# Performance work log

Measured on AMD Instinct MI355X. Metric: run time of the kernel, lower is better.

Reference implementation:

```python
import jax, jax.numpy as jnp
import numpy as np

N = 30000   # nodes
E = 600000  # edges
IN = 256    # in_channels
HID = 128   # 2*out_channels
OUT = 64    # out_channels


def setup_inputs() -> dict:
    key = jax.random.key(0)
    k = jax.random.split(key, 6)
    x = jax.random.normal(k[0], (N, IN), dtype=jnp.float32)
    edge_index = jax.random.randint(k[1], (2, E), 0, N, dtype=jnp.int64)
    W1 = jax.random.normal(k[2], (IN, HID), dtype=jnp.float32) * (1.0 / np.sqrt(IN))
    b1 = jnp.zeros((HID,), dtype=jnp.float32)
    W2 = jax.random.normal(k[3], (HID, OUT), dtype=jnp.float32) * (1.0 / np.sqrt(HID))
    b2 = jnp.zeros((OUT,), dtype=jnp.float32)
    return {"x": x, "edge_index": edge_index, "W1": W1, "b1": b1, "W2": W2, "b2": b2}


def _gcn_norm(edge_index, n_nodes):
    # PyG gcn_norm with add_self_loops=True, edge_weight=1
    loop = jnp.arange(n_nodes, dtype=edge_index.dtype)
    src = jnp.concatenate([edge_index[0], loop])
    dst = jnp.concatenate([edge_index[1], loop])
    deg = jax.ops.segment_sum(jnp.ones_like(dst, dtype=jnp.float32), dst,
                              num_segments=n_nodes)
    dinv = jnp.where(deg > 0, jax.lax.rsqrt(deg), 0.0)
    norm = dinv[src] * dinv[dst]  # [E+N]
    return src, dst, norm


def _gcn_conv(h, src, dst, norm, W, b, n_nodes):
    h = h @ W                              # [N, out] linear first (PyG order)
    msg = h[src] * norm[:, None]           # gather + per-edge scale, [E+N, out]
    out = jax.ops.segment_sum(msg, dst, num_segments=n_nodes)  # scatter-add
    return out + b


def reference(x, edge_index, W1, b1, W2, b2):
    n_nodes = x.shape[0]
    src, dst, norm = _gcn_norm(edge_index, n_nodes)
    h = _gcn_conv(x, src, dst, norm, W1, b1, n_nodes)
    h = jax.nn.relu(h)
    return _gcn_conv(h, src, dst, norm, W2, b2, n_nodes)
```

## Files before the change

kernel.cpp:

```cpp
#include <hip/hip_runtime.h>


#define GCN_IN 256
#define GCN_HID 128
#define GCN_OUT 64

#define BKT 128
#define SBE 4096
#define SRCM 0x1FFFFFFu

typedef unsigned short ushort_t;
typedef __attribute__((ext_vector_type(8))) short short8;
typedef __attribute__((ext_vector_type(8))) unsigned short ushort8;
typedef __attribute__((ext_vector_type(4))) float f32x4;

__device__ inline float bf2f(ushort_t u) {
  union { unsigned int i; float f; } x; x.i = ((unsigned int)u) << 16; return x.f;
}
__device__ inline ushort_t f2bf(float f) {
  union { float f; unsigned int i; } u; u.f = f;
  unsigned int r = u.i + 0x7FFFu + ((u.i >> 16) & 1u);
  return (ushort_t)(r >> 16);
}

__global__ void probe_kernel(const ushort_t* __restrict__ xu,
                             const int* __restrict__ ei,
                             int* __restrict__ flags) {
  int lane = threadIdx.x;
  int c = 0, nz = 0;
  for (int i = lane; i < 128; i += 64) {
    ushort_t u = xu[2 * i];
    int e = (u >> 7) & 0xFF;
    c += (e >= 100 && e <= 140) ? 1 : 0;
    nz += (ei[2 * i + 1] != 0) ? 1 : 0;
  }
  for (int off = 32; off > 0; off >>= 1) {
    c += __shfl_down(c, off);
    nz += __shfl_down(nz, off);
  }
  if (lane == 0) {
    flags[0] = (c >= 64) ? 0 : 1;
    flags[1] = (nz == 0) ? 1 : 0;
  }
}

__global__ void hist_kernel(const int* __restrict__ ei, int E,
                            int* __restrict__ Hmat, int nsb, int nbin,
                            const int* __restrict__ flags) {
  __shared__ int hist[256];
  int t = threadIdx.x;
  int sb = blockIdx.x;
  hist[t] = 0;
  __syncthreads();
  int base = sb * SBE;
  int end = base + SBE; if (end > E) end = E;
  bool i64 = flags[1] != 0;
  for (int i = base + t; i < end; i += 256) {
    int d = i64 ? ei[2 * E + 2 * i] : ei[E + i];
    atomicAdd(&hist[d >> 7], 1);
  }
  __syncthreads();
  for (int b = t; b < nbin; b += 256)
    Hmat[b * nsb + sb] = hist[b];
}

__global__ void scanA_kernel(const int* __restrict__ Hmat, int nsb,
                             int* __restrict__ binsum) {
  __shared__ int red[256];
  int t = threadIdx.x;
  const int* row = Hmat + (size_t)blockIdx.x * nsb;
  int s = 0;
  for (int i = t; i < nsb; i += 256) s += row[i];
  red[t] = s;
  __syncthreads();
  for (int off = 128; off > 0; off >>= 1) {
    if (t < off) red[t] += red[t + off];
    __syncthreads();
  }
  if (t == 0) binsum[blockIdx.x] = red[0];
}

__global__ void scanC_kernel(int* __restrict__ Hmat, int nsb,
                             const int* __restrict__ binsum, int nbin) {
  __shared__ int bred[256];
  __shared__ int red[256];
  int t = threadIdx.x;
  int bs = (t < nbin) ? binsum[t] : 0;
  bred[t] = bs;
  __syncthreads();
  for (int off = 1; off < 256; off <<= 1) {
    int u = (t >= off) ? bred[t - off] : 0;
    __syncthreads();
    bred[t] += u;
    __syncthreads();
  }
  __shared__ int seed_sh;
  if (t == (int)blockIdx.x) seed_sh = bred[t] - bs;
  __syncthreads();
  int seed = seed_sh;
  int* row = Hmat + (size_t)blockIdx.x * nsb;
  int self = (t < nsb) ? row[t] : 0;
  red[t] = self;
  __syncthreads();
  for (int off = 1; off < 256; off <<= 1) {
    int u = (t >= off) ? red[t - off] : 0;
    __syncthreads();
    red[t] += u;
    __syncthreads();
  }
  if (t < nsb) row[t] = seed + red[t] - self;
}

__global__ void stage2_kernel(const int* __restrict__ ei, int E,
                              const int* __restrict__ Hscan, int nsb, int nbin,
                              unsigned int* __restrict__ stage,
                              const int* __restrict__ flags) {
  __shared__ int cur[256];
  int t = threadIdx.x;
  int sb = blockIdx.x;
  for (int b = t; b < nbin; b += 256)
    cur[b] = Hscan[b * nsb + sb];
  __syncthreads();
  int base = sb * SBE;
  int end = base + SBE; if (end > E) end = E;
  bool i64 = flags[1] != 0;
  for (int i = base + t; i < end; i += 256) {
    int s, d;
    if (i64) { s = ei[2 * i]; d = ei[2 * E + 2 * i]; }
    else     { s = ei[i];     d = ei[E + i]; }
    int pos = atomicAdd(&cur[d >> 7], 1);
    stage[pos] = (unsigned int)s | ((unsigned int)(d & 127) << 25);
  }
}

__global__ void scatter_kernel(const unsigned int* __restrict__ stage,
                               const int* __restrict__ Hmat, int nsb, int nbin,
                               int* __restrict__ csr_src,
                               int* __restrict__ row_ptr,
                               float* __restrict__ dinv, int n, int E) {
  __shared__ int lcnt[BKT];
  __shared__ int lscan[BKT];
  __shared__ int lcur[BKT];
  const int t = threadIdx.x;
  const int b = blockIdx.x;
  const int node0 = b * BKT;
  const int nn = (n - node0 < BKT) ? (n - node0) : BKT;
  const int rb = Hmat[b * nsb];
  const int re = (b + 1 < nbin) ? Hmat[(b + 1) * nsb] : E;
  if (t < BKT) lcnt[t] = 0;
  __syncthreads();
  for (int i = rb + t; i < re; i += 256)
    atomicAdd(&lcnt[stage[i] >> 25], 1);
  __syncthreads();
  if (t < BKT) lscan[t] = lcnt[t];
  __syncthreads();
  for (int off = 1; off < BKT; off <<= 1) {
    int v = 0;
    if (t < BKT && t >= off) v = lscan[t - off];
    __syncthreads();
    if (t < BKT) lscan[t] += v;
    __syncthreads();
  }
  if (t < BKT) {
    int excl = rb + lscan[t] - lcnt[t];
    lcur[t] = excl;
    if (t < nn) {
      row_ptr[node0 + t] = excl;
      dinv[node0 + t] = rsqrtf((float)(lcnt[t] + 1));
    }
  }
  if (t == 0 && node0 + nn == n) row_ptr[n] = E;
  __syncthreads();
  for (int i = rb + t; i < re; i += 256) {
    unsigned int p = stage[i];
    int l = p >> 25;
    int pos = atomicAdd(&lcur[l], 1);
    csr_src[pos] = (int)(p & SRCM);
  }
}

__global__ void prep_w_kernel(const void* __restrict__ W1, const void* __restrict__ W2,
                              ushort_t* __restrict__ Wt1, ushort_t* __restrict__ Wt2,
                              const int* __restrict__ flags) {
  int i = blockIdx.x * blockDim.x + threadIdx.x;
  bool f32 = flags[0] != 0;
  if (i < GCN_IN * GCN_HID) {
    int k = i >> 7, n = i & 127;
    float v = f32 ? ((const float*)W1)[i] : bf2f(((const ushort_t*)W1)[i]);
    Wt1[n * GCN_IN + k] = f2bf(v);
  }
  int j = i - GCN_IN * GCN_HID;
  if (j >= 0 && j < GCN_HID * GCN_OUT) {
    int k = j >> 6, n = j & 63;
    float v = f32 ? ((const float*)W2)[j] : bf2f(((const ushort_t*)W2)[j]);
    Wt2[n * GCN_HID + k] = f2bf(v);
  }
}

template<int K, int NC, int A_MODE>
__global__ __launch_bounds__(256)
void gemm_mfma_kernel(const void* __restrict__ A, const ushort_t* __restrict__ Bt,
                      ushort_t* __restrict__ C, int M, const int* __restrict__ flags) {
  constexpr int KT = 32;
  constexpr int NT = NC / 32;
  __shared__ ushort_t As[32 * KT];
  __shared__ ushort_t Bs[NC * KT];
  const int tid = threadIdx.x;
  const int wv = tid >> 6;
  const int lane = tid & 63;
  const int ml = lane & 15;
  const int quad = lane >> 4;
  const int row0 = blockIdx.x * 32;
  const int mrow = (wv & 1) * 16 + ml;
  const int ncol0 = (wv >> 1) * (NC / 2);
  const bool aF32 = (A_MODE == 0) && (flags[0] != 0);
  f32x4 acc[NT] = {};

  for (int kt = 0; kt < K; kt += KT) {
    for (int c = tid; c < 32 * KT / 8; c += 256) {
      int r = c >> 2, cq = c & 3;
      ushort8 o;
      if (row0 + r < M) {
        if (aF32) {
          const float* ap = (const float*)A + (size_t)(row0 + r) * K + kt + cq * 8;
          float4 f0 = *(const float4*)ap;
          float4 f1 = *(const float4*)(ap + 4);
          o[0] = f2bf(f0.x); o[1] = f2bf(f0.y); o[2] = f2bf(f0.z); o[3] = f2bf(f0.w);
          o[4] = f2bf(f1.x); o[5] = f2bf(f1.y); o[6] = f2bf(f1.z); o[7] = f2bf(f1.w);
        } else {
          o = *(const ushort8*)((const ushort_t*)A + (size_t)(row0 + r) * K + kt + cq * 8);
        }
      } else {
        o = (ushort8)0;
      }
      *(ushort8*)&As[c * 8] = o;
    }
    for (int c = tid; c < NC * KT / 8; c += 256) {
      int n = c >> 2, cq = c & 3;
      *(ushort8*)&Bs[c * 8] = *(const ushort8*)(Bt + (size_t)n * K + kt + cq * 8);
    }
    __syncthreads();
    short8 af = *(const short8*)&As[mrow * KT + quad * 8];
#pragma unroll
    for (int t = 0; t < NT; ++t) {
      short8 bf = *(const short8*)&Bs[(ncol0 + t * 16 + ml) * KT + quad * 8];
      acc[t] = __builtin_amdgcn_mfma_f32_16x16x32_bf16(af, bf, acc[t], 0, 0, 0);
    }
    __syncthreads();
  }

  const int orow = row0 + (wv & 1) * 16 + quad * 4;
#pragma unroll
  for (int t = 0; t < NT; ++t) {
    int col = ncol0 + t * 16 + ml;
#pragma unroll
    for (int r = 0; r < 4; ++r) {
      if (orow + r < M)
        C[(size_t)(orow + r) * NC + col] = f2bf(acc[t][r]);
    }
  }
}


__global__ void aggregate_relu_kernel(const ushort_t* __restrict__ h,
                                      const int* __restrict__ row_ptr,
                                      const int* __restrict__ csr_src,
                                      const float* __restrict__ dinv,
                                      const void* __restrict__ bias,
                                      ushort_t* __restrict__ outp, int n,
                                      const int* __restrict__ flags) {
  int wave = threadIdx.x >> 6;
  int lane = threadIdx.x & 63;
  int v = blockIdx.x * (blockDim.x >> 6) + wave;
  if (v >= n) return;
  const int q = lane & 15, g = lane >> 4;
  float acc[8] = {};
  int beg = row_ptr[v], end = row_ptr[v + 1];
  for (int base = beg; base < end; base += 64) {
    int navail = end - base; if (navail > 64) navail = 64;
    int sv = 0; float dv = 0.f;
    if (base + lane < end) { sv = csr_src[base + lane]; dv = dinv[sv]; }
    for (int j = 0; j < navail; j += 4) {
      int e = j + g;
      int s = __shfl(sv, e);
      float ds = __shfl(dv, e);
      ushort8 hv = *(const ushort8*)(h + (size_t)s * GCN_HID + q * 8);
#pragma unroll
      for (int k = 0; k < 8; ++k) acc[k] = fmaf(ds, bf2f(hv[k]), acc[k]);
    }
  }
#pragma unroll
  for (int k = 0; k < 8; ++k) {
    acc[k] += __shfl_xor(acc[k], 16);
    acc[k] += __shfl_xor(acc[k], 32);
  }
  if (g == 0) {
    float di = dinv[v];
    float sl = di * di;
    ushort8 hv = *(const ushort8*)(h + (size_t)v * GCN_HID + q * 8);
    const bool bF32 = flags[0] != 0;
    ushort8 o;
#pragma unroll
    for (int k = 0; k < 8; ++k) {
      float bv = bF32 ? ((const float*)bias)[q * 8 + k]
                      : bf2f(((const ushort_t*)bias)[q * 8 + k]);
      o[k] = f2bf(fmaxf(di * acc[k] + sl * bf2f(hv[k]) + bv, 0.f));
    }
    *(ushort8*)(outp + (size_t)v * GCN_HID + q * 8) = o;
  }
}

__global__ void aggregate_out_kernel(const ushort_t* __restrict__ h,
                                     const int* __restrict__ row_ptr,
                                     const int* __restrict__ csr_src,
                                     const float* __restrict__ dinv,
                                     const void* __restrict__ bias,
                                     void* __restrict__ outp, int n,
                                     const int* __restrict__ flags) {
  int wave = threadIdx.x >> 6;
  int lane = threadIdx.x & 63;
  int v = blockIdx.x * (blockDim.x >> 6) + wave;
  if (v >= n) return;
  const int q = lane & 7, g = lane >> 3;
  float acc[8] = {};
  int beg = row_ptr[v], end = row_ptr[v + 1];
  for (int base = beg; base < end; base += 64) {
    int navail = end - base; if (navail > 64) navail = 64;
    int sv = 0; float dv = 0.f;
    if (base + lane < end) { sv = csr_src[base + lane]; dv = dinv[sv]; }
    for (int j = 0; j < navail; j += 8) {
      int e = j + g;
      int s = __shfl(sv, e);
      float ds = __shfl(dv, e);
      ushort8 hv = *(const ushort8*)(h + (size_t)s * GCN_OUT + q * 8);
#pragma unroll
      for (int k = 0; k < 8; ++k) acc[k] = fmaf(ds, bf2f(hv[k]), acc[k]);
    }
  }
#pragma unroll
  for (int k = 0; k < 8; ++k) {
    acc[k] += __shfl_xor(acc[k], 8);
    acc[k] += __shfl_xor(acc[k], 16);
    acc[k] += __shfl_xor(acc[k], 32);
  }
  if (g == 0) {
    float di = dinv[v];
    float sl = di * di;
    ushort8 hv = *(const ushort8*)(h + (size_t)v * GCN_OUT + q * 8);
    const bool oF32 = flags[0] != 0;
    float r[8];
#pragma unroll
    for (int k = 0; k < 8; ++k) {
      float bv = oF32 ? ((const float*)bias)[q * 8 + k]
                      : bf2f(((const ushort_t*)bias)[q * 8 + k]);
      r[k] = di * acc[k] + sl * bf2f(hv[k]) + bv;
    }
    if (oF32) {
      float* op = (float*)outp + (size_t)v * GCN_OUT + q * 8;
      *(float4*)op = make_float4(r[0], r[1], r[2], r[3]);
      *(float4*)(op + 4) = make_float4(r[4], r[5], r[6], r[7]);
    } else {
      ushort8 o;
#pragma unroll
      for (int k = 0; k < 8; ++k) o[k] = f2bf(r[k]);
      *(ushort8*)((ushort_t*)outp + (size_t)v * GCN_OUT + q * 8) = o;
    }
  }
}


extern "C" void kernel_launch(void* const* d_in, const int* in_sizes, int n_in,
                              void* d_out, int out_size, void* d_ws, size_t ws_size,
                              hipStream_t stream) {
  const void* x  = d_in[0];
  const int*  ei = (const int*)d_in[1];
  const void* W1 = d_in[2];
  const void* b1 = d_in[3];
  const void* W2 = d_in[4];
  const void* b2 = d_in[5];

  const int N = in_sizes[0] / GCN_IN;
  const int E = in_sizes[1] / 2;
  const int nsb  = (E + SBE - 1) / SBE;
  const int nbin = (N + BKT - 1) / BKT;

  size_t off = 0;
  auto alloc = [&](size_t bytes) -> void* {
    void* p = (char*)d_ws + off;
    off += (bytes + 255) & ~(size_t)255;
    return p;
  };
  int*          flags   = (int*)alloc(256);
  int*          binsum  = (int*)alloc(256 * 4);
  int*          Hmat    = (int*)alloc((size_t)nbin * nsb * 4);
  unsigned int* stage   = (unsigned int*)alloc((size_t)E * 4);
  int*          csr_src = (int*)alloc((size_t)E * 4);
  int*          row_ptr = (int*)alloc((size_t)(N + 1) * 4);
  float*        dinv    = (float*)alloc((size_t)N * 4);
  ushort_t*     h1      = (ushort_t*)alloc((size_t)N * GCN_HID * 2);
  ushort_t*     hag     = (ushort_t*)alloc((size_t)N * GCN_HID * 2);
  ushort_t*     wt1     = (ushort_t*)alloc((size_t)GCN_HID * GCN_IN * 2);
  ushort_t*     wt2     = (ushort_t*)alloc((size_t)GCN_OUT * GCN_HID * 2);
  ushort_t*     h2      = h1;

  probe_kernel<<<1, 64, 0, stream>>>((const ushort_t*)x, ei, flags);
  hist_kernel<<<nsb, 256, 0, stream>>>(ei, E, Hmat, nsb, nbin, flags);
  scanA_kernel<<<nbin, 256, 0, stream>>>(Hmat, nsb, binsum);
  scanC_kernel<<<nbin, 256, 0, stream>>>(Hmat, nsb, binsum, nbin);
  stage2_kernel<<<nsb, 256, 0, stream>>>(ei, E, Hmat, nsb, nbin, stage, flags);
  scatter_kernel<<<nbin, 256, 0, stream>>>(stage, Hmat, nsb, nbin, csr_src,
                                           row_ptr, dinv, N, E);

  prep_w_kernel<<<(GCN_IN * GCN_HID + GCN_HID * GCN_OUT + 255) / 256, 256, 0, stream>>>(
      W1, W2, wt1, wt2, flags);

  gemm_mfma_kernel<GCN_IN, GCN_HID, 0>
      <<<(N + 31) / 32, 256, 0, stream>>>(x, wt1, h1, N, flags);

  int gAgg = (N + 3) / 4;
  aggregate_relu_kernel<<<gAgg, 256, 0, stream>>>(h1, row_ptr, csr_src,
                                                  dinv, b1, hag, N, flags);

  gemm_mfma_kernel<GCN_HID, GCN_OUT, 2>
      <<<(N + 31) / 32, 256, 0, stream>>>(hag, wt2, h2, N, flags);

  aggregate_out_kernel<<<gAgg, 256, 0, stream>>>(h2, row_ptr, csr_src,
                                                 dinv, b2, d_out, N, flags);
}
```

Before: 177.1 us.

## Fold dtype probes into consumers, merge scan kernels, swizzle GEMM LDS, unroll gathers

Removes the separate probe kernel: each kernel that needs the int64 or fp32 check now recomputes it inline, with the fp32 check moved into prep_w using W1. The two scan kernels are merged into one that recomputes bin sums per block and writes a separate Hscan buffer. The GEMM now stages K in chunks of up to 128 with an XOR-swizzled LDS layout, cutting the number of barriers. Both aggregation loops are unrolled to issue four independent gathers per step for more memory-level parallelism. The trade-off is redundant per-block probe and bin-sum work plus higher register pressure in the aggregation kernels.

```diff
diff --git a/kernel.cpp b/kernel.cpp
--- a/kernel.cpp
+++ b/kernel.cpp
@@ -23,38 +23,20 @@
   return (ushort_t)(r >> 16);
 }
 
-__global__ void probe_kernel(const ushort_t* __restrict__ xu,
-                             const int* __restrict__ ei,
-                             int* __restrict__ flags) {
-  int lane = threadIdx.x;
-  int c = 0, nz = 0;
-  for (int i = lane; i < 128; i += 64) {
-    ushort_t u = xu[2 * i];
-    int e = (u >> 7) & 0xFF;
-    c += (e >= 100 && e <= 140) ? 1 : 0;
-    nz += (ei[2 * i + 1] != 0) ? 1 : 0;
-  }
-  for (int off = 32; off > 0; off >>= 1) {
-    c += __shfl_down(c, off);
-    nz += __shfl_down(nz, off);
-  }
-  if (lane == 0) {
-    flags[0] = (c >= 64) ? 0 : 1;
-    flags[1] = (nz == 0) ? 1 : 0;
-  }
-}
-
 __global__ void hist_kernel(const int* __restrict__ ei, int E,
-                            int* __restrict__ Hmat, int nsb, int nbin,
-                            const int* __restrict__ flags) {
+                            int* __restrict__ Hmat, int nsb, int nbin) {
   __shared__ int hist[256];
+  __shared__ int nzc;
   int t = threadIdx.x;
   int sb = blockIdx.x;
   hist[t] = 0;
-  __syncthreads();
+  if (t == 0) nzc = 0;
+  __syncthreads();
+  if (t < 128 && ei[2 * t + 1] != 0) atomicAdd(&nzc, 1);
+  __syncthreads();
+  bool i64 = (nzc == 0);
   int base = sb * SBE;
   int end = base + SBE; if (end > E) end = E;
-  bool i64 = flags[1] != 0;
   for (int i = base + t; i < end; i += 256) {
     int d = i64 ? ei[2 * E + 2 * i] : ei[E + i];
     atomicAdd(&hist[d >> 7], 1);
@@ -64,28 +46,17 @@
     Hmat[b * nsb + sb] = hist[b];
 }
 
-__global__ void scanA_kernel(const int* __restrict__ Hmat, int nsb,
-                             int* __restrict__ binsum) {
-  __shared__ int red[256];
-  int t = threadIdx.x;
-  const int* row = Hmat + (size_t)blockIdx.x * nsb;
-  int s = 0;
-  for (int i = t; i < nsb; i += 256) s += row[i];
-  red[t] = s;
-  __syncthreads();
-  for (int off = 128; off > 0; off >>= 1) {
-    if (t < off) red[t] += red[t + off];
-    __syncthreads();
-  }
-  if (t == 0) binsum[blockIdx.x] = red[0];
-}
-
-__global__ void scanC_kernel(int* __restrict__ Hmat, int nsb,
-                             const int* __restrict__ binsum, int nbin) {
+__global__ void scanAC_kernel(const int* __restrict__ Hmat,
+                              int* __restrict__ Hscan, int nsb, int nbin) {
   __shared__ int bred[256];
   __shared__ int red[256];
+  __shared__ int seed_sh;
   int t = threadIdx.x;
-  int bs = (t < nbin) ? binsum[t] : 0;
+  int bs = 0;
+  if (t < nbin) {
+    const int* row = Hmat + (size_t)t * nsb;
+    for (int i = 0; i < nsb; ++i) bs += row[i];
+  }
   bred[t] = bs;
   __syncthreads();
   for (int off = 1; off < 256; off <<= 1) {
@@ -94,11 +65,10 @@
     bred[t] += u;
     __syncthreads();
   }
-  __shared__ int seed_sh;
   if (t == (int)blockIdx.x) seed_sh = bred[t] - bs;
   __syncthreads();
   int seed = seed_sh;
-  int* row = Hmat + (size_t)blockIdx.x * nsb;
+  const int* row = Hmat + (size_t)blockIdx.x * nsb;
   int self = (t < nsb) ? row[t] : 0;
   red[t] = self;
   __syncthreads();
@@ -108,22 +78,25 @@
     red[t] += u;
     __syncthreads();
   }
-  if (t < nsb) row[t] = seed + red[t] - self;
+  if (t < nsb) Hscan[(size_t)blockIdx.x * nsb + t] = seed + red[t] - self;
 }
 
 __global__ void stage2_kernel(const int* __restrict__ ei, int E,
                               const int* __restrict__ Hscan, int nsb, int nbin,
-                              unsigned int* __restrict__ stage,
-                              const int* __restrict__ flags) {
+                              unsigned int* __restrict__ stage) {
   __shared__ int cur[256];
+  __shared__ int nzc;
   int t = threadIdx.x;
   int sb = blockIdx.x;
+  if (t == 0) nzc = 0;
+  __syncthreads();
+  if (t < 128 && ei[2 * t + 1] != 0) atomicAdd(&nzc, 1);
   for (int b = t; b < nbin; b += 256)
     cur[b] = Hscan[b * nsb + sb];
   __syncthreads();
+  bool i64 = (nzc == 0);
   int base = sb * SBE;
   int end = base + SBE; if (end > E) end = E;
-  bool i64 = flags[1] != 0;
   for (int i = base + t; i < end; i += 256) {
     int s, d;
     if (i64) { s = ei[2 * i]; d = ei[2 * E + 2 * i]; }
@@ -134,7 +107,7 @@
 }
 
 __global__ void scatter_kernel(const unsigned int* __restrict__ stage,
-                               const int* __restrict__ Hmat, int nsb, int nbin,
+                               const int* __restrict__ Hscan, int nsb, int nbin,
                                int* __restrict__ csr_src,
                                int* __restrict__ row_ptr,
                                float* __restrict__ dinv, int n, int E) {
@@ -145,8 +118,8 @@
   const int b = blockIdx.x;
   const int node0 = b * BKT;
   const int nn = (n - node0 < BKT) ? (n - node0) : BKT;
-  const int rb = Hmat[b * nsb];
-  const int re = (b + 1 < nbin) ? Hmat[(b + 1) * nsb] : E;
+  const int rb = Hscan[b * nsb];
+  const int re = (b + 1 < nbin) ? Hscan[(b + 1) * nsb] : E;
   if (t < BKT) lcnt[t] = 0;
   __syncthreads();
   for (int i = rb + t; i < re; i += 256)
@@ -181,9 +154,20 @@
 
 __global__ void prep_w_kernel(const void* __restrict__ W1, const void* __restrict__ W2,
                               ushort_t* __restrict__ Wt1, ushort_t* __restrict__ Wt2,
-                              const int* __restrict__ flags) {
+                              int* __restrict__ flags) {
+  __shared__ int csh;
+  if (threadIdx.x == 0) csh = 0;
+  __syncthreads();
+  if (threadIdx.x < 128) {
+    ushort_t u = ((const ushort_t*)W1)[2 * threadIdx.x];
+    int e = (u >> 7) & 0xFF;
+    if (e >= 100 && e <= 140) atomicAdd(&csh, 1);
+  }
+  __syncthreads();
+  bool f32 = (csh < 64);
+  if (blockIdx.x == 0 && threadIdx.x == 0) flags[0] = f32 ? 1 : 0;
+
   int i = blockIdx.x * blockDim.x + threadIdx.x;
-  bool f32 = flags[0] != 0;
   if (i < GCN_IN * GCN_HID) {
     int k = i >> 7, n = i & 127;
     float v = f32 ? ((const float*)W1)[i] : bf2f(((const ushort_t*)W1)[i]);
@@ -201,10 +185,11 @@
 __global__ __launch_bounds__(256)
 void gemm_mfma_kernel(const void* __restrict__ A, const ushort_t* __restrict__ Bt,
                       ushort_t* __restrict__ C, int M, const int* __restrict__ flags) {
-  constexpr int KT = 32;
+  constexpr int KH = (K > 128) ? 128 : K;
+  constexpr int KPC = KH / 8;
   constexpr int NT = NC / 32;
-  __shared__ ushort_t As[32 * KT];
-  __shared__ ushort_t Bs[NC * KT];
+  __shared__ ushort_t As[32 * KH];
+  __shared__ ushort_t Bs[NC * KH];
   const int tid = threadIdx.x;
   const int wv = tid >> 6;
   const int lane = tid & 63;
@@ -216,37 +201,46 @@
   const bool aF32 = (A_MODE == 0) && (flags[0] != 0);
   f32x4 acc[NT] = {};
 
-  for (int kt = 0; kt < K; kt += KT) {
-    for (int c = tid; c < 32 * KT / 8; c += 256) {
-      int r = c >> 2, cq = c & 3;
+  for (int ch = 0; ch < K; ch += KH) {
+    if (ch) __syncthreads();
+    for (int c = tid; c < 32 * KPC; c += 256) {
+      int r = c / KPC, cq = c % KPC;
       ushort8 o;
       if (row0 + r < M) {
         if (aF32) {
-          const float* ap = (const float*)A + (size_t)(row0 + r) * K + kt + cq * 8;
+          const float* ap = (const float*)A + (size_t)(row0 + r) * K + ch + cq * 8;
           float4 f0 = *(const float4*)ap;
           float4 f1 = *(const float4*)(ap + 4);
           o[0] = f2bf(f0.x); o[1] = f2bf(f0.y); o[2] = f2bf(f0.z); o[3] = f2bf(f0.w);
           o[4] = f2bf(f1.x); o[5] = f2bf(f1.y); o[6] = f2bf(f1.z); o[7] = f2bf(f1.w);
         } else {
-          o = *(const ushort8*)((const ushort_t*)A + (size_t)(row0 + r) * K + kt + cq * 8);
+          o = *(const ushort8*)((const ushort_t*)A + (size_t)(row0 + r) * K + ch + cq * 8);
         }
       } else {
         o = (ushort8)0;
       }
-      *(ushort8*)&As[c * 8] = o;
-    }
-    for (int c = tid; c < NC * KT / 8; c += 256) {
-      int n = c >> 2, cq = c & 3;
-      *(ushort8*)&Bs[c * 8] = *(const ushort8*)(Bt + (size_t)n * K + kt + cq * 8);
-    }
-    __syncthreads();
-    short8 af = *(const short8*)&As[mrow * KT + quad * 8];
-#pragma unroll
-    for (int t = 0; t < NT; ++t) {
-      short8 bf = *(const short8*)&Bs[(ncol0 + t * 16 + ml) * KT + quad * 8];
-      acc[t] = __builtin_amdgcn_mfma_f32_16x16x32_bf16(af, bf, acc[t], 0, 0, 0);
-    }
-    __syncthreads();
+      int byte = (cq * 16) ^ ((r & 7) << 4);
+      *(ushort8*)((char*)As + r * (KH * 2) + byte) = o;
+    }
+    for (int c = tid; c < NC * KPC; c += 256) {
+      int nr = c / KPC, cq = c % KPC;
+      ushort8 o = *(const ushort8*)(Bt + (size_t)nr * K + ch + cq * 8);
+      int byte = (cq * 16) ^ ((nr & 7) << 4);
+      *(ushort8*)((char*)Bs + nr * (KH * 2) + byte) = o;
+    }
+    __syncthreads();
+#pragma unroll
+    for (int kt = 0; kt < KH; kt += 32) {
+      int abyte = (kt * 2 + quad * 16) ^ ((mrow & 7) << 4);
+      short8 af = *(const short8*)((const char*)As + mrow * (KH * 2) + abyte);
+#pragma unroll
+      for (int t = 0; t < NT; ++t) {
+        int nr = ncol0 + t * 16 + ml;
+        int bbyte = (kt * 2 + quad * 16) ^ ((nr & 7) << 4);
+        short8 bf = *(const short8*)((const char*)Bs + nr * (KH * 2) + bbyte);
+        acc[t] = __builtin_amdgcn_mfma_f32_16x16x32_bf16(af, bf, acc[t], 0, 0, 0);
+      }
+    }
   }
 
   const int orow = row0 + (wv & 1) * 16 + quad * 4;
@@ -280,13 +274,27 @@
     int navail = end - base; if (navail > 64) navail = 64;
     int sv = 0; float dv = 0.f;
     if (base + lane < end) { sv = csr_src[base + lane]; dv = dinv[sv]; }
-    for (int j = 0; j < navail; j += 4) {
-      int e = j + g;
-      int s = __shfl(sv, e);
-      float ds = __shfl(dv, e);
-      ushort8 hv = *(const ushort8*)(h + (size_t)s * GCN_HID + q * 8);
-#pragma unroll
-      for (int k = 0; k < 8; ++k) acc[k] = fmaf(ds, bf2f(hv[k]), acc[k]);
+#pragma unroll
+    for (int j = 0; j < 64; j += 16) {
+      if (j >= navail) break;
+      int e0 = j + g, e1 = j + 4 + g, e2 = j + 8 + g, e3 = j + 12 + g;
+      int s0 = __shfl(sv, e0), s1 = __shfl(sv, e1);
+      int s2 = __shfl(sv, e2), s3 = __shfl(sv, e3);
+      float d0 = __shfl(dv, e0), d1 = __shfl(dv, e1);
+      float d2 = __shfl(dv, e2), d3 = __shfl(dv, e3);
+      bool p1 = e1 < navail, p2 = e2 < navail, p3 = e3 < navail;
+      ushort8 hv0 = (ushort8)0, hv1 = (ushort8)0, hv2 = (ushort8)0, hv3 = (ushort8)0;
+      if (e0 < navail) hv0 = *(const ushort8*)(h + (size_t)s0 * GCN_HID + q * 8);
+      if (p1) hv1 = *(const ushort8*)(h + (size_t)s1 * GCN_HID + q * 8);
+      if (p2) hv2 = *(const ushort8*)(h + (size_t)s2 * GCN_HID + q * 8);
+      if (p3) hv3 = *(const ushort8*)(h + (size_t)s3 * GCN_HID + q * 8);
+#pragma unroll
+      for (int k = 0; k < 8; ++k) {
+        acc[k] = fmaf(d0, bf2f(hv0[k]), acc[k]);
+        acc[k] = fmaf(d1, bf2f(hv1[k]), acc[k]);
+        acc[k] = fmaf(d2, bf2f(hv2[k]), acc[k]);
+        acc[k] = fmaf(d3, bf2f(hv3[k]), acc[k]);
+      }
     }
   }
 #pragma unroll
@@ -328,13 +336,27 @@
     int navail = end - base; if (navail > 64) navail = 64;
     int sv = 0; float dv = 0.f;
     if (base + lane < end) { sv = csr_src[base + lane]; dv = dinv[sv]; }
-    for (int j = 0; j < navail; j += 8) {
-      int e = j + g;
-      int s = __shfl(sv, e);
-      float ds = __shfl(dv, e);
-      ushort8 hv = *(const ushort8*)(h + (size_t)s * GCN_OUT + q * 8);
-#pragma unroll
-      for (int k = 0; k < 8; ++k) acc[k] = fmaf(ds, bf2f(hv[k]), acc[k]);
+#pragma unroll
+    for (int j = 0; j < 64; j += 32) {
+      if (j >= navail) break;
+      int e0 = j + g, e1 = j + 8 + g, e2 = j + 16 + g, e3 = j + 24 + g;
+      int s0 = __shfl(sv, e0), s1 = __shfl(sv, e1);
+      int s2 = __shfl(sv, e2), s3 = __shfl(sv, e3);
+      float d0 = __shfl(dv, e0), d1 = __shfl(dv, e1);
+      float d2 = __shfl(dv, e2), d3 = __shfl(dv, e3);
+      bool p1 = e1 < navail, p2 = e2 < navail, p3 = e3 < navail;
+      ushort8 hv0 = (ushort8)0, hv1 = (ushort8)0, hv2 = (ushort8)0, hv3 = (ushort8)0;
+      if (e0 < navail) hv0 = *(const ushort8*)(h + (size_t)s0 * GCN_OUT + q * 8);
+      if (p1) hv1 = *(const ushort8*)(h + (size_t)s1 * GCN_OUT + q * 8);
+      if (p2) hv2 = *(const ushort8*)(h + (size_t)s2 * GCN_OUT + q * 8);
+      if (p3) hv3 = *(const ushort8*)(h + (size_t)s3 * GCN_OUT + q * 8);
+#pragma unroll
+      for (int k = 0; k < 8; ++k) {
+        acc[k] = fmaf(d0, bf2f(hv0[k]), acc[k]);
+        acc[k] = fmaf(d1, bf2f(hv1[k]), acc[k]);
+        acc[k] = fmaf(d2, bf2f(hv2[k]), acc[k]);
+        acc[k] = fmaf(d3, bf2f(hv3[k]), acc[k]);
+      }
     }
   }
 #pragma unroll
@@ -391,8 +413,8 @@
     return p;
   };
   int*          flags   = (int*)alloc(256);
-  int*          binsum  = (int*)alloc(256 * 4);
   int*          Hmat    = (int*)alloc((size_t)nbin * nsb * 4);
+  int*          Hscan   = (int*)alloc((size_t)nbin * nsb * 4);
   unsigned int* stage   = (unsigned int*)alloc((size_t)E * 4);
   int*          csr_src = (int*)alloc((size_t)E * 4);
   int*          row_ptr = (int*)alloc((size_t)(N + 1) * 4);
@@ -403,16 +425,14 @@
   ushort_t*     wt2     = (ushort_t*)alloc((size_t)GCN_OUT * GCN_HID * 2);
   ushort_t*     h2      = h1;
 
-  probe_kernel<<<1, 64, 0, stream>>>((const ushort_t*)x, ei, flags);
-  hist_kernel<<<nsb, 256, 0, stream>>>(ei, E, Hmat, nsb, nbin, flags);
-  scanA_kernel<<<nbin, 256, 0, stream>>>(Hmat, nsb, binsum);
-  scanC_kernel<<<nbin, 256, 0, stream>>>(Hmat, nsb, binsum, nbin);
-  stage2_kernel<<<nsb, 256, 0, stream>>>(ei, E, Hmat, nsb, nbin, stage, flags);
-  scatter_kernel<<<nbin, 256, 0, stream>>>(stage, Hmat, nsb, nbin, csr_src,
-                                           row_ptr, dinv, N, E);
-
   prep_w_kernel<<<(GCN_IN * GCN_HID + GCN_HID * GCN_OUT + 255) / 256, 256, 0, stream>>>(
       W1, W2, wt1, wt2, flags);
+
+  hist_kernel<<<nsb, 256, 0, stream>>>(ei, E, Hmat, nsb, nbin);
+  scanAC_kernel<<<nbin, 256, 0, stream>>>(Hmat, Hscan, nsb, nbin);
+  stage2_kernel<<<nsb, 256, 0, stream>>>(ei, E, Hscan, nsb, nbin, stage);
+  scatter_kernel<<<nbin, 256, 0, stream>>>(stage, Hscan, nsb, nbin, csr_src,
+                                           row_ptr, dinv, N, E);
 
   gemm_mfma_kernel<GCN_IN, GCN_HID, 0>
       <<<(N + 31) / 32, 256, 0, stream>>>(x, wt1, h1, N, flags);
```

Result: slower. 192.9 us (+8.9%).
